# Performance work log

Hardware: AMD Instinct MI355X
Metric: run time of the kernel (lower is better)

The kernel has to match this reference:

```python
import jax, jax.numpy as jnp
import numpy as np

N_PTS = 131072
IN_CH = 63
IN_CH_VIEWS = 27
WIDTH = 256
NUM_HEADS = 4
SCALE = 0.05


def setup_inputs() -> dict:
    key = jax.random.key(0)
    ks = jax.random.split(key, 12)
    H, W = NUM_HEADS, WIDTH
    inp = {
        'x': jax.random.normal(ks[0], (N_PTS, IN_CH + IN_CH_VIEWS), jnp.float32),
        'head_idx': jax.random.randint(ks[1], (N_PTS,), 0, NUM_HEADS),
        # shared trunk: layer0 63->256, layers1..3 256->256 (no skip before split_at=4)
        'W0': jax.random.normal(ks[2], (IN_CH, W), jnp.float32) * SCALE,
        'b0': jnp.zeros((W,), jnp.float32),
        'Ws': jax.random.normal(ks[3], (3, W, W), jnp.float32) * SCALE,
        'bs': jnp.zeros((3, W), jnp.float32),
        # per-head tails: g=4 in skips -> (W+63)->W, then g=5..7 W->W
        'tW0': jax.random.normal(ks[4], (H, W + IN_CH, W), jnp.float32) * SCALE,
        'tb0': jnp.zeros((H, W), jnp.float32),
        'tWs': jax.random.normal(ks[5], (H, 3, W, W), jnp.float32) * SCALE,
        'tbs': jnp.zeros((H, 3, W), jnp.float32),
        # per-head viewdirs output heads
        'featW': jax.random.normal(ks[6], (H, W, W), jnp.float32) * SCALE,
        'featb': jnp.zeros((H, W), jnp.float32),
        'alphaW': jax.random.normal(ks[7], (H, W, 1), jnp.float32) * SCALE,
        'alphab': jnp.zeros((H, 1), jnp.float32),
        'viewsW': jax.random.normal(ks[8], (H, IN_CH_VIEWS + W, W // 2), jnp.float32) * SCALE,
        'viewsb': jnp.zeros((H, W // 2), jnp.float32),
        'rgbW': jax.random.normal(ks[9], (H, W // 2, 3), jnp.float32) * SCALE,
        'rgbb': jnp.zeros((H, 3), jnp.float32),
    }
    return inp


def reference(x, head_idx, W0, b0, Ws, bs, tW0, tb0, tWs, tbs,
              featW, featb, alphaW, alphab, viewsW, viewsb, rgbW, rgbb):
    input_pts = x[:, :IN_CH]          # [N, 63]
    input_views = x[:, IN_CH:]        # [N, 27]

    # shared trunk (layers 0..3, no skip hits in this range)
    h = jax.nn.relu(input_pts @ W0 + b0)
    for i in range(Ws.shape[0]):
        h = jax.nn.relu(h @ Ws[i] + bs[i])

    # per-head tails, computed densely for ALL heads (as in the original)
    # first tail layer g=4 is a skip layer: concat input_pts
    ht = jnp.concatenate([input_pts, h], axis=-1)          # [N, 319]
    ha = jax.nn.relu(jnp.einsum('nf,hfo->nho', ht, tW0) + tb0[None])  # [N, H, 256]
    for j in range(tWs.shape[1]):
        ha = jax.nn.relu(jnp.einsum('nho,hop->nhp', ha, tWs[:, j]) + tbs[None, :, j])

    # per-head viewdir output heads
    alpha = jnp.einsum('nho,hop->nhp', ha, alphaW) + alphab[None]     # [N, H, 1]
    feat = jnp.einsum('nho,hop->nhp', ha, featW) + featb[None]        # [N, H, 256]
    views_b = jnp.broadcast_to(input_views[:, None, :], (x.shape[0], feat.shape[1], IN_CH_VIEWS))
    hv = jnp.concatenate([feat, views_b], axis=-1)                    # [N, H, 283]
    hv = jax.nn.relu(jnp.einsum('nho,hop->nhp', hv, viewsW) + viewsb[None])
    rgb = jnp.einsum('nho,hop->nhp', hv, rgbW) + rgbb[None]           # [N, H, 3]

    outs = jnp.concatenate([rgb, alpha], axis=-1)                     # [N, H, 4]
    sel = jnp.take_along_axis(outs, head_idx[:, None, None], axis=1)[:, 0]  # [N, 4]
    return sel
```

## Files before the change

### kernel.cpp

```cpp
#include <hip/hip_runtime.h>

#define N_PTS 131072
#define TILE 64
#define THREADS 512

typedef __bf16 bf16;
typedef __bf16 bf16x8 __attribute__((ext_vector_type(8)));
typedef float f32x4 __attribute__((ext_vector_type(4)));

#define WS_PERM_OFF   256
#define WS_WPACK_OFF  (256 + N_PTS * 4)
#define OFF_W0     0
#define OFF_WS     16384
#define OFF_TW0    212992
#define OFF_TWS    540672
#define OFF_FEATW  1327104
#define OFF_VIEWSW 1589248
#define TOTAL_PACK 1736704

#define PTS_BASE 0
#define H_BASE   8192
#define LDS_BYTES 40960

__device__ __forceinline__ unsigned swz(unsigned base, unsigned row, unsigned rowstride,
                                        unsigned kbyte) {
  return (base + row * rowstride + kbyte) ^ ((row & 7u) << 4);
}

__global__ void k_pack(const float* __restrict__ W0, const float* __restrict__ Ws,
                       const float* __restrict__ tW0, const float* __restrict__ tWs,
                       const float* __restrict__ featW, const float* __restrict__ viewsW,
                       bf16* __restrict__ out) {
  for (int idx = blockIdx.x * blockDim.x + threadIdx.x; idx < TOTAL_PACK;
       idx += gridDim.x * blockDim.x) {
    float v;
    if (idx < OFF_WS) {
      int o = idx >> 6, k = idx & 63;
      v = (k < 63) ? W0[k * 256 + o] : 0.f;
    } else if (idx < OFF_TW0) {
      int i = idx - OFF_WS; int l = i >> 16, r = i & 65535, o = r >> 8, k = r & 255;
      v = Ws[l * 65536 + k * 256 + o];
    } else if (idx < OFF_TWS) {
      int i = idx - OFF_TW0; int h = i / 81920, r = i % 81920, o = r / 320, k = r % 320;
      v = (k < 63) ? tW0[(h * 319 + k) * 256 + o]
                   : (k == 63 ? 0.f : tW0[(h * 319 + k - 1) * 256 + o]);
    } else if (idx < OFF_FEATW) {
      int i = idx - OFF_TWS; int hj = i >> 16, r = i & 65535, o = r >> 8, k = r & 255;
      v = tWs[(hj * 256 + k) * 256 + o];
    } else if (idx < OFF_VIEWSW) {
      int i = idx - OFF_FEATW; int h = i >> 16, r = i & 65535, o = r >> 8, k = r & 255;
      v = featW[(h * 256 + k) * 256 + o];
    } else {
      int i = idx - OFF_VIEWSW; int h = i / 36864, r = i % 36864, o = r / 288, k = r % 288;
      v = (k < 283) ? viewsW[(h * 283 + k) * 128 + o] : 0.f;
    }
    out[idx] = (bf16)v;
  }
}

__global__ void k_zero(int* c) { if (threadIdx.x < 64) c[threadIdx.x] = 0; }

__global__ void k_count(const int* __restrict__ head, int* __restrict__ c) {
  __shared__ int lc[4];
  if (threadIdx.x < 4) lc[threadIdx.x] = 0;
  __syncthreads();
  int p = blockIdx.x * 256 + threadIdx.x;
  if (p < N_PTS) atomicAdd(&lc[head[p]], 1);
  __syncthreads();
  if (threadIdx.x < 4 && lc[threadIdx.x]) atomicAdd(&c[threadIdx.x], lc[threadIdx.x]);
}

__global__ void k_scan(int* c) {
  c[8] = 0; c[24] = 0;
  for (int h = 0; h < 4; ++h) {
    c[8 + h + 1] = c[8 + h] + c[h];
    c[16 + h] = c[8 + h];
    c[24 + h + 1] = c[24 + h] + (c[h] + TILE - 1) / TILE;
  }
}

__global__ void k_scatter(const int* __restrict__ head, int* __restrict__ c,
                          int* __restrict__ perm) {
  int p = blockIdx.x * 256 + threadIdx.x;
  int h = (p < N_PTS) ? head[p] : -1;
  int lane = threadIdx.x & 63;
  #pragma unroll
  for (int hh = 0; hh < 4; ++hh) {
    unsigned long long m = __ballot(h == hh);
    if (m == 0ull) continue;
    int leader = __builtin_ctzll(m);
    int base = 0;
    if (lane == leader) base = atomicAdd(&c[16 + hh], __popcll(m));
    base = __shfl(base, leader);
    if (h == hh) {
      int rank = __popcll(m & ((1ull << lane) - 1ull));
      perm[base + rank] = p;
    }
  }
}

template <int NFRAG, bool RELU, int A0KC, int A1KC>
__device__ __forceinline__ void mfma_layer(char* lds, const bf16* __restrict__ Wt, int wK,
                                           const float* __restrict__ bias,
                                           int a0_base, int a0_stride,
                                           int a1_base, int a1_stride,
                                           int out_base, int out_stride,
                                           int lane, int wave) {
  const int l15 = lane & 15, l4 = lane >> 4;
  constexpr int KC = A0KC + A1KC;
  f32x4 acc[4][NFRAG];
  #pragma unroll
  for (int m = 0; m < 4; ++m)
    #pragma unroll
    for (int n = 0; n < NFRAG; ++n) acc[m][n] = (f32x4){0.f, 0.f, 0.f, 0.f};

  const int c0 = wave * (NFRAG * 16);
  const bf16* bbase[NFRAG];
  #pragma unroll
  for (int n = 0; n < NFRAG; ++n)
    bbase[n] = Wt + (c0 + n * 16 + l15) * wK + l4 * 8;

  bf16x8 bcur[NFRAG];
  #pragma unroll
  for (int n = 0; n < NFRAG; ++n) bcur[n] = *(const bf16x8*)(bbase[n]);

  #pragma unroll 1
  for (int kc = 0; kc < KC; ++kc) {
    const int kn = (kc + 1 < KC) ? kc + 1 : kc;
    bf16x8 bnext[NFRAG];
    #pragma unroll
    for (int n = 0; n < NFRAG; ++n) bnext[n] = *(const bf16x8*)(bbase[n] + kn * 32);

    const int base   = (kc < A0KC) ? a0_base   : a1_base;
    const int stride = (kc < A0KC) ? a0_stride : a1_stride;
    const int kl     = ((kc < A0KC) ? kc : kc - A0KC) * 32;
    bf16x8 a[4];
    #pragma unroll
    for (int m = 0; m < 4; ++m)
      a[m] = *(const bf16x8*)(lds + swz(base, m * 16 + l15, stride, (kl + l4 * 8) * 2));

    #pragma unroll
    for (int n = 0; n < NFRAG; ++n)
      #pragma unroll
      for (int m = 0; m < 4; ++m)
        acc[m][n] = __builtin_amdgcn_mfma_f32_16x16x32_bf16(a[m], bcur[n], acc[m][n], 0, 0, 0);

    #pragma unroll
    for (int n = 0; n < NFRAG; ++n) bcur[n] = bnext[n];
  }
  __syncthreads();
  #pragma unroll
  for (int n = 0; n < NFRAG; ++n) {
    int col = c0 + n * 16 + l15;
    float bv = bias[col];
    #pragma unroll
    for (int m = 0; m < 4; ++m) {
      #pragma unroll
      for (int j = 0; j < 4; ++j) {
        float v = acc[m][n][j] + bv;
        if (RELU) v = fmaxf(v, 0.f);
        int row = m * 16 + l4 * 4 + j;
        *(bf16*)(lds + swz(out_base, row, out_stride, col * 2)) = (bf16)v;
      }
    }
  }
  __syncthreads();
}

__global__ __launch_bounds__(THREADS, 4) void k_main(
    const float* __restrict__ x, const int* __restrict__ ctrl, const int* __restrict__ perm,
    const bf16* __restrict__ wpack,
    const float* __restrict__ b0, const float* __restrict__ bs,
    const float* __restrict__ tb0p, const float* __restrict__ tbsp,
    const float* __restrict__ featb, const float* __restrict__ alphaW,
    const float* __restrict__ alphab, const float* __restrict__ viewsb,
    const float* __restrict__ rgbW, const float* __restrict__ rgbb,
    float* __restrict__ outp) {
  __shared__ __attribute__((aligned(16))) char lds[LDS_BYTES];
  __shared__ int pidx[TILE];
  __shared__ float alpha_s[TILE];

  const int tid = threadIdx.x;
  const int lane = tid & 63, wave = tid >> 6;

  const int tbA = ctrl[24], tbB = ctrl[25], tbC = ctrl[26], tbD = ctrl[27], tbE = ctrl[28];
  const int bid = blockIdx.x;
  if (bid >= tbE) return;
  const int hh = (bid >= tbB) + (bid >= tbC) + (bid >= tbD);
  const int tb_h = (hh == 0) ? tbA : ((hh == 1) ? tbB : ((hh == 2) ? tbC : tbD));
  const int start = ctrl[8 + hh] + (bid - tb_h) * TILE;
  const int nv = min(TILE, ctrl[8 + hh + 1] - start);

  if (tid < TILE) pidx[tid] = (tid < nv) ? perm[start + tid] : -1;
  __syncthreads();

  for (int i = tid; i < TILE * 64; i += THREADS) {
    int row = i >> 6, c = i & 63;
    int p = pidx[row];
    float v = (p >= 0 && c < 63) ? x[p * 90 + c] : 0.f;
    *(bf16*)(lds + swz(PTS_BASE, row, 128, c * 2)) = (bf16)v;
  }
  __syncthreads();

  const bf16* W0p    = wpack + OFF_W0;
  const bf16* Wsp    = wpack + OFF_WS;
  const bf16* tW0p   = wpack + OFF_TW0 + hh * 81920;
  const bf16* tWsp   = wpack + OFF_TWS + hh * 3 * 65536;
  const bf16* featWp = wpack + OFF_FEATW + hh * 65536;
  const bf16* viewsWp= wpack + OFF_VIEWSW + hh * 36864;

  mfma_layer<2, true, 2, 0>(lds, W0p, 64, b0, PTS_BASE, 128, 0, 0, H_BASE, 512, lane, wave);
  for (int i = 0; i < 3; ++i)
    mfma_layer<2, true, 8, 0>(lds, Wsp + i * 65536, 256, bs + i * 256,
                              H_BASE, 512, 0, 0, H_BASE, 512, lane, wave);
  mfma_layer<2, true, 2, 8>(lds, tW0p, 320, tb0p + hh * 256,
                            PTS_BASE, 128, H_BASE, 512, H_BASE, 512, lane, wave);

  for (int i = tid; i < TILE * 32; i += THREADS) {
    int row = i >> 5, c = i & 31;
    int p = pidx[row];
    float v = (p >= 0 && c < 27) ? x[p * 90 + 63 + c] : 0.f;
    *(bf16*)(lds + swz(PTS_BASE, row, 128, c * 2)) = (bf16)v;
  }

  for (int j = 0; j < 3; ++j)
    mfma_layer<2, true, 8, 0>(lds, tWsp + j * 65536, 256, tbsp + (hh * 3 + j) * 256,
                              H_BASE, 512, 0, 0, H_BASE, 512, lane, wave);

  if (wave < 4) {
    int p = wave * 16 + (lane & 15);
    int kq = lane >> 4;
    const float* aW = alphaW + hh * 256;
    float s = 0.f;
    for (int i = 0; i < 8; ++i) {
      int k = kq * 64 + i * 8;
      bf16x8 hv8 = *(const bf16x8*)(lds + swz(H_BASE, p, 512, k * 2));
      #pragma unroll
      for (int j = 0; j < 8; ++j) s += (float)hv8[j] * aW[k + j];
    }
    s += __shfl_xor(s, 16);
    s += __shfl_xor(s, 32);
    if (kq == 0) alpha_s[p] = s + alphab[hh];
  }
  __syncthreads();

  mfma_layer<2, false, 8, 0>(lds, featWp, 256, featb + hh * 256,
                             H_BASE, 512, 0, 0, H_BASE, 512, lane, wave);
  mfma_layer<1, true, 8, 1>(lds, viewsWp, 288, viewsb + hh * 128,
                            H_BASE, 512, PTS_BASE, 128, H_BASE, 512, lane, wave);

  if (wave < 4) {
    int p = wave * 16 + (lane & 15);
    int kq = lane >> 4;
    const float* rW = rgbW + hh * 128 * 3;
    float r0 = 0.f, r1 = 0.f, r2 = 0.f;
    for (int i = 0; i < 4; ++i) {
      int k = kq * 32 + i * 8;
      bf16x8 hv8 = *(const bf16x8*)(lds + swz(H_BASE, p, 512, k * 2));
      #pragma unroll
      for (int j = 0; j < 8; ++j) {
        float hvf = (float)hv8[j];
        r0 += hvf * rW[(k + j) * 3 + 0];
        r1 += hvf * rW[(k + j) * 3 + 1];
        r2 += hvf * rW[(k + j) * 3 + 2];
      }
    }
    r0 += __shfl_xor(r0, 16); r0 += __shfl_xor(r0, 32);
    r1 += __shfl_xor(r1, 16); r1 += __shfl_xor(r1, 32);
    r2 += __shfl_xor(r2, 16); r2 += __shfl_xor(r2, 32);
    if (kq == 0 && p < nv) {
      int pt = pidx[p];
      float4 o = make_float4(r0 + rgbb[hh * 3 + 0], r1 + rgbb[hh * 3 + 1],
                             r2 + rgbb[hh * 3 + 2], alpha_s[p]);
      *(float4*)(outp + pt * 4) = o;
    }
  }
}

extern "C" void kernel_launch(void* const* d_in, const int* in_sizes, int n_in,
                              void* d_out, int out_size, void* d_ws, size_t ws_size,
                              hipStream_t stream) {
  const float* x      = (const float*)d_in[0];
  const int*   head   = (const int*)d_in[1];
  const float* W0     = (const float*)d_in[2];
  const float* b0     = (const float*)d_in[3];
  const float* Ws     = (const float*)d_in[4];
  const float* bs     = (const float*)d_in[5];
  const float* tW0    = (const float*)d_in[6];
  const float* tb0    = (const float*)d_in[7];
  const float* tWs    = (const float*)d_in[8];
  const float* tbs    = (const float*)d_in[9];
  const float* featW  = (const float*)d_in[10];
  const float* featb  = (const float*)d_in[11];
  const float* alphaW = (const float*)d_in[12];
  const float* alphab = (const float*)d_in[13];
  const float* viewsW = (const float*)d_in[14];
  const float* viewsb = (const float*)d_in[15];
  const float* rgbW   = (const float*)d_in[16];
  const float* rgbb   = (const float*)d_in[17];

  int*  ctrl  = (int*)d_ws;
  int*  perm  = (int*)((char*)d_ws + WS_PERM_OFF);
  bf16* wpack = (bf16*)((char*)d_ws + WS_WPACK_OFF);

  k_pack<<<2048, 256, 0, stream>>>(W0, Ws, tW0, tWs, featW, viewsW, wpack);
  k_zero<<<1, 64, 0, stream>>>(ctrl);
  k_count<<<N_PTS / 256, 256, 0, stream>>>(head, ctrl);
  k_scan<<<1, 1, 0, stream>>>(ctrl);
  k_scatter<<<N_PTS / 256, 256, 0, stream>>>(head, ctrl, perm);
  k_main<<<N_PTS / TILE + 4, THREADS, 0, stream>>>(x, ctrl, perm, wpack,
                                                   b0, bs, tb0, tbs, featb, alphaW, alphab,
                                                   viewsb, rgbW, rgbb, (float*)d_out);
}
```

Before: 470.9 us.

## Ping-pong activation buffers to drop per-layer barrier and deepen weight prefetch

Activations now alternate between two LDS buffers, so each layer reads from one and writes the other. This lets the barrier between the MFMA loop and the epilogue store, plus the one after the alpha pass, be removed. Weight fragment prefetch is deepened from one k-step ahead to two. The zero kernel is folded into the pack kernel to save a launch. LDS use grows from 40 KB to 72 KB per block, which may lower occupancy, and the extra prefetch registers add register pressure.

Result: slower. 568.9 us (+20.8%).

```diff
diff --git a/kernel.cpp b/kernel.cpp
--- a/kernel.cpp
+++ b/kernel.cpp
@@ -19,8 +19,9 @@
 #define TOTAL_PACK 1736704
 
 #define PTS_BASE 0
-#define H_BASE   8192
-#define LDS_BYTES 40960
+#define HA_BASE  8192
+#define HB_BASE  40960
+#define LDS_BYTES 73728
 
 __device__ __forceinline__ unsigned swz(unsigned base, unsigned row, unsigned rowstride,
                                         unsigned kbyte) {
@@ -30,7 +31,8 @@
 __global__ void k_pack(const float* __restrict__ W0, const float* __restrict__ Ws,
                        const float* __restrict__ tW0, const float* __restrict__ tWs,
                        const float* __restrict__ featW, const float* __restrict__ viewsW,
-                       bf16* __restrict__ out) {
+                       bf16* __restrict__ out, int* __restrict__ ctrl) {
+  if (blockIdx.x == 0 && threadIdx.x < 64) ctrl[threadIdx.x] = 0;
   for (int idx = blockIdx.x * blockDim.x + threadIdx.x; idx < TOTAL_PACK;
        idx += gridDim.x * blockDim.x) {
     float v;
@@ -58,8 +60,6 @@
   }
 }
 
-__global__ void k_zero(int* c) { if (threadIdx.x < 64) c[threadIdx.x] = 0; }
-
 __global__ void k_count(const int* __restrict__ head, int* __restrict__ c) {
   __shared__ int lc[4];
   if (threadIdx.x < 4) lc[threadIdx.x] = 0;
@@ -115,21 +115,22 @@
     for (int n = 0; n < NFRAG; ++n) acc[m][n] = (f32x4){0.f, 0.f, 0.f, 0.f};
 
   const int c0 = wave * (NFRAG * 16);
-  const bf16* bbase[NFRAG];
-  #pragma unroll
-  for (int n = 0; n < NFRAG; ++n)
-    bbase[n] = Wt + (c0 + n * 16 + l15) * wK + l4 * 8;
-
-  bf16x8 bcur[NFRAG];
-  #pragma unroll
-  for (int n = 0; n < NFRAG; ++n) bcur[n] = *(const bf16x8*)(bbase[n]);
+  const bf16* bp = Wt + (c0 + l15) * wK + l4 * 8;
+  const int nstep = 16 * wK;
+
+  bf16x8 bc[NFRAG], bn[NFRAG];
+  #pragma unroll
+  for (int n = 0; n < NFRAG; ++n) bc[n] = *(const bf16x8*)(bp + n * nstep);
+  constexpr int K1 = (KC > 1) ? 32 : 0;
+  #pragma unroll
+  for (int n = 0; n < NFRAG; ++n) bn[n] = *(const bf16x8*)(bp + n * nstep + K1);
 
   #pragma unroll 1
   for (int kc = 0; kc < KC; ++kc) {
-    const int kn = (kc + 1 < KC) ? kc + 1 : kc;
-    bf16x8 bnext[NFRAG];
-    #pragma unroll
-    for (int n = 0; n < NFRAG; ++n) bnext[n] = *(const bf16x8*)(bbase[n] + kn * 32);
+    const int kf = (kc + 2 < KC) ? kc + 2 : KC - 1;
+    bf16x8 bf_[NFRAG];
+    #pragma unroll
+    for (int n = 0; n < NFRAG; ++n) bf_[n] = *(const bf16x8*)(bp + n * nstep + kf * 32);
 
     const int base   = (kc < A0KC) ? a0_base   : a1_base;
     const int stride = (kc < A0KC) ? a0_stride : a1_stride;
@@ -143,12 +144,12 @@
     for (int n = 0; n < NFRAG; ++n)
       #pragma unroll
       for (int m = 0; m < 4; ++m)
-        acc[m][n] = __builtin_amdgcn_mfma_f32_16x16x32_bf16(a[m], bcur[n], acc[m][n], 0, 0, 0);
-
-    #pragma unroll
-    for (int n = 0; n < NFRAG; ++n) bcur[n] = bnext[n];
-  }
-  __syncthreads();
+        acc[m][n] = __builtin_amdgcn_mfma_f32_16x16x32_bf16(a[m], bc[n], acc[m][n], 0, 0, 0);
+
+    #pragma unroll
+    for (int n = 0; n < NFRAG; ++n) { bc[n] = bn[n]; bn[n] = bf_[n]; }
+  }
+
   #pragma unroll
   for (int n = 0; n < NFRAG; ++n) {
     int col = c0 + n * 16 + l15;
@@ -209,12 +210,12 @@
   const bf16* featWp = wpack + OFF_FEATW + hh * 65536;
   const bf16* viewsWp= wpack + OFF_VIEWSW + hh * 36864;
 
-  mfma_layer<2, true, 2, 0>(lds, W0p, 64, b0, PTS_BASE, 128, 0, 0, H_BASE, 512, lane, wave);
-  for (int i = 0; i < 3; ++i)
-    mfma_layer<2, true, 8, 0>(lds, Wsp + i * 65536, 256, bs + i * 256,
-                              H_BASE, 512, 0, 0, H_BASE, 512, lane, wave);
+  mfma_layer<2, true, 2, 0>(lds, W0p, 64, b0, PTS_BASE, 128, 0, 0, HA_BASE, 512, lane, wave);
+  mfma_layer<2, true, 8, 0>(lds, Wsp,           256, bs,       HA_BASE, 512, 0, 0, HB_BASE, 512, lane, wave);
+  mfma_layer<2, true, 8, 0>(lds, Wsp + 65536,   256, bs + 256, HB_BASE, 512, 0, 0, HA_BASE, 512, lane, wave);
+  mfma_layer<2, true, 8, 0>(lds, Wsp + 131072,  256, bs + 512, HA_BASE, 512, 0, 0, HB_BASE, 512, lane, wave);
   mfma_layer<2, true, 2, 8>(lds, tW0p, 320, tb0p + hh * 256,
-                            PTS_BASE, 128, H_BASE, 512, H_BASE, 512, lane, wave);
+                            PTS_BASE, 128, HB_BASE, 512, HA_BASE, 512, lane, wave);
 
   for (int i = tid; i < TILE * 32; i += THREADS) {
     int row = i >> 5, c = i & 31;
@@ -223,9 +224,9 @@
     *(bf16*)(lds + swz(PTS_BASE, row, 128, c * 2)) = (bf16)v;
   }
 
-  for (int j = 0; j < 3; ++j)
-    mfma_layer<2, true, 8, 0>(lds, tWsp + j * 65536, 256, tbsp + (hh * 3 + j) * 256,
-                              H_BASE, 512, 0, 0, H_BASE, 512, lane, wave);
+  mfma_layer<2, true, 8, 0>(lds, tWsp,          256, tbsp + hh * 768,       HA_BASE, 512, 0, 0, HB_BASE, 512, lane, wave);
+  mfma_layer<2, true, 8, 0>(lds, tWsp + 65536,  256, tbsp + hh * 768 + 256, HB_BASE, 512, 0, 0, HA_BASE, 512, lane, wave);
+  mfma_layer<2, true, 8, 0>(lds, tWsp + 131072, 256, tbsp + hh * 768 + 512, HA_BASE, 512, 0, 0, HB_BASE, 512, lane, wave);
 
   if (wave < 4) {
     int p = wave * 16 + (lane & 15);
@@ -234,7 +235,7 @@
     float s = 0.f;
     for (int i = 0; i < 8; ++i) {
       int k = kq * 64 + i * 8;
-      bf16x8 hv8 = *(const bf16x8*)(lds + swz(H_BASE, p, 512, k * 2));
+      bf16x8 hv8 = *(const bf16x8*)(lds + swz(HB_BASE, p, 512, k * 2));
       #pragma unroll
       for (int j = 0; j < 8; ++j) s += (float)hv8[j] * aW[k + j];
     }
@@ -242,12 +243,11 @@
     s += __shfl_xor(s, 32);
     if (kq == 0) alpha_s[p] = s + alphab[hh];
   }
-  __syncthreads();
 
   mfma_layer<2, false, 8, 0>(lds, featWp, 256, featb + hh * 256,
-                             H_BASE, 512, 0, 0, H_BASE, 512, lane, wave);
+                             HB_BASE, 512, 0, 0, HA_BASE, 512, lane, wave);
   mfma_layer<1, true, 8, 1>(lds, viewsWp, 288, viewsb + hh * 128,
-                            H_BASE, 512, PTS_BASE, 128, H_BASE, 512, lane, wave);
+                            HA_BASE, 512, PTS_BASE, 128, HB_BASE, 512, lane, wave);
 
   if (wave < 4) {
     int p = wave * 16 + (lane & 15);
@@ -256,7 +256,7 @@
     float r0 = 0.f, r1 = 0.f, r2 = 0.f;
     for (int i = 0; i < 4; ++i) {
       int k = kq * 32 + i * 8;
-      bf16x8 hv8 = *(const bf16x8*)(lds + swz(H_BASE, p, 512, k * 2));
+      bf16x8 hv8 = *(const bf16x8*)(lds + swz(HB_BASE, p, 512, k * 2));
       #pragma unroll
       for (int j = 0; j < 8; ++j) {
         float hvf = (float)hv8[j];
@@ -303,8 +303,7 @@
   int*  perm  = (int*)((char*)d_ws + WS_PERM_OFF);
   bf16* wpack = (bf16*)((char*)d_ws + WS_WPACK_OFF);
 
-  k_pack<<<2048, 256, 0, stream>>>(W0, Ws, tW0, tWs, featW, viewsW, wpack);
-  k_zero<<<1, 64, 0, stream>>>(ctrl);
+  k_pack<<<2048, 256, 0, stream>>>(W0, Ws, tW0, tWs, featW, viewsW, wpack, ctrl);
   k_count<<<N_PTS / 256, 256, 0, stream>>>(head, ctrl);
   k_scan<<<1, 1, 0, stream>>>(ctrl);
   k_scatter<<<N_PTS / 256, 256, 0, stream>>>(head, ctrl, perm);
```

## Stage weight tiles into double-buffered LDS via global_load_lds; fuse head count into pack

Applied to the files above, without the earlier changes.

Each MFMA layer now stages its weight K-slices into a double-buffered LDS region with direct global-to-LDS loads, using an XOR swizzle. Waves read their B fragments from LDS instead of holding prefetched fragments in registers, which removes register-side global loads and register pressure. The cost is a block-wide barrier per K step, and LDS per block grows from 40 KB to 72 KB, which may lower the number of resident blocks per CU. Separately, the head-count pass is folded into the weight-pack kernel and the zero kernel becomes a memset, removing two small launches.

Result: faster. 440.6 us (-6.4%).

```diff
diff --git a/kernel.cpp b/kernel.cpp
--- a/kernel.cpp
+++ b/kernel.cpp
@@ -20,19 +20,32 @@
 
 #define PTS_BASE 0
 #define H_BASE   8192
-#define LDS_BYTES 40960
+#define B_BASE   40960
+#define LDS_BYTES 73728
 
 __device__ __forceinline__ unsigned swz(unsigned base, unsigned row, unsigned rowstride,
                                         unsigned kbyte) {
   return (base + row * rowstride + kbyte) ^ ((row & 7u) << 4);
 }
 
+__device__ __forceinline__ void gload_lds16(const bf16* g, char* l) {
+  __builtin_amdgcn_global_load_lds(
+      (const __attribute__((address_space(1))) void*)g,
+      (__attribute__((address_space(3))) void*)l, 16, 0, 0);
+}
+
 __global__ void k_pack(const float* __restrict__ W0, const float* __restrict__ Ws,
                        const float* __restrict__ tW0, const float* __restrict__ tWs,
                        const float* __restrict__ featW, const float* __restrict__ viewsW,
-                       bf16* __restrict__ out) {
-  for (int idx = blockIdx.x * blockDim.x + threadIdx.x; idx < TOTAL_PACK;
-       idx += gridDim.x * blockDim.x) {
+                       bf16* __restrict__ out, const int* __restrict__ head,
+                       int* __restrict__ ctrl) {
+  __shared__ int lc[4];
+  if (threadIdx.x < 4) lc[threadIdx.x] = 0;
+  __syncthreads();
+  int gid = blockIdx.x * blockDim.x + threadIdx.x;
+  if (gid < N_PTS) atomicAdd(&lc[head[gid]], 1);
+
+  for (int idx = gid; idx < TOTAL_PACK; idx += gridDim.x * blockDim.x) {
     float v;
     if (idx < OFF_WS) {
       int o = idx >> 6, k = idx & 63;
@@ -56,18 +69,8 @@
     }
     out[idx] = (bf16)v;
   }
-}
-
-__global__ void k_zero(int* c) { if (threadIdx.x < 64) c[threadIdx.x] = 0; }
-
-__global__ void k_count(const int* __restrict__ head, int* __restrict__ c) {
-  __shared__ int lc[4];
-  if (threadIdx.x < 4) lc[threadIdx.x] = 0;
-  __syncthreads();
-  int p = blockIdx.x * 256 + threadIdx.x;
-  if (p < N_PTS) atomicAdd(&lc[head[p]], 1);
-  __syncthreads();
-  if (threadIdx.x < 4 && lc[threadIdx.x]) atomicAdd(&c[threadIdx.x], lc[threadIdx.x]);
+  __syncthreads();
+  if (threadIdx.x < 4 && lc[threadIdx.x]) atomicAdd(&ctrl[threadIdx.x], lc[threadIdx.x]);
 }
 
 __global__ void k_scan(int* c) {
@@ -99,7 +102,21 @@
   }
 }
 
-template <int NFRAG, bool RELU, int A0KC, int A1KC>
+template <int OUTS>
+__device__ __forceinline__ void stage_B(const bf16* __restrict__ Wt, int wK, int kk,
+                                        char* lds, int bufsel, int wave, int lane) {
+  constexpr int ISSUES = OUTS / 128;
+  #pragma unroll
+  for (int s = 0; s < ISSUES; ++s) {
+    int reg = wave * ISSUES + s;
+    int o = reg * 16 + (lane >> 2);
+    int j = lane & 3;
+    const bf16* g = Wt + o * wK + kk + ((j ^ (o & 3)) << 3);
+    gload_lds16(g, lds + B_BASE + bufsel * 16384 + reg * 1024);
+  }
+}
+
+template <int NFRAG, bool RELU, int A0KC, int A1KC, int OUTS>
 __device__ __forceinline__ void mfma_layer(char* lds, const bf16* __restrict__ Wt, int wK,
                                            const float* __restrict__ bias,
                                            int a0_base, int a0_stride,
@@ -115,21 +132,14 @@
     for (int n = 0; n < NFRAG; ++n) acc[m][n] = (f32x4){0.f, 0.f, 0.f, 0.f};
 
   const int c0 = wave * (NFRAG * 16);
-  const bf16* bbase[NFRAG];
-  #pragma unroll
-  for (int n = 0; n < NFRAG; ++n)
-    bbase[n] = Wt + (c0 + n * 16 + l15) * wK + l4 * 8;
-
-  bf16x8 bcur[NFRAG];
-  #pragma unroll
-  for (int n = 0; n < NFRAG; ++n) bcur[n] = *(const bf16x8*)(bbase[n]);
+
+  stage_B<OUTS>(Wt, wK, 0, lds, 0, wave, lane);
+  __syncthreads();
 
   #pragma unroll 1
   for (int kc = 0; kc < KC; ++kc) {
-    const int kn = (kc + 1 < KC) ? kc + 1 : kc;
-    bf16x8 bnext[NFRAG];
-    #pragma unroll
-    for (int n = 0; n < NFRAG; ++n) bnext[n] = *(const bf16x8*)(bbase[n] + kn * 32);
+    const int buf = kc & 1;
+    if (kc + 1 < KC) stage_B<OUTS>(Wt, wK, (kc + 1) * 32, lds, buf ^ 1, wave, lane);
 
     const int base   = (kc < A0KC) ? a0_base   : a1_base;
     const int stride = (kc < A0KC) ? a0_stride : a1_stride;
@@ -139,16 +149,22 @@
     for (int m = 0; m < 4; ++m)
       a[m] = *(const bf16x8*)(lds + swz(base, m * 16 + l15, stride, (kl + l4 * 8) * 2));
 
+    bf16x8 b[NFRAG];
+    #pragma unroll
+    for (int n = 0; n < NFRAG; ++n) {
+      int col = c0 + n * 16 + l15;
+      b[n] = *(const bf16x8*)(lds + B_BASE + buf * 16384 + col * 64 + ((l4 ^ (col & 3)) << 4));
+    }
+
     #pragma unroll
     for (int n = 0; n < NFRAG; ++n)
       #pragma unroll
       for (int m = 0; m < 4; ++m)
-        acc[m][n] = __builtin_amdgcn_mfma_f32_16x16x32_bf16(a[m], bcur[n], acc[m][n], 0, 0, 0);
-
-    #pragma unroll
-    for (int n = 0; n < NFRAG; ++n) bcur[n] = bnext[n];
-  }
-  __syncthreads();
+        acc[m][n] = __builtin_amdgcn_mfma_f32_16x16x32_bf16(a[m], b[n], acc[m][n], 0, 0, 0);
+
+    __syncthreads();
+  }
+
   #pragma unroll
   for (int n = 0; n < NFRAG; ++n) {
     int col = c0 + n * 16 + l15;
@@ -164,7 +180,6 @@
       }
     }
   }
-  __syncthreads();
 }
 
 __global__ __launch_bounds__(THREADS, 4) void k_main(
@@ -200,7 +215,6 @@
     float v = (p >= 0 && c < 63) ? x[p * 90 + c] : 0.f;
     *(bf16*)(lds + swz(PTS_BASE, row, 128, c * 2)) = (bf16)v;
   }
-  __syncthreads();
 
   const bf16* W0p    = wpack + OFF_W0;
   const bf16* Wsp    = wpack + OFF_WS;
@@ -209,12 +223,12 @@
   const bf16* featWp = wpack + OFF_FEATW + hh * 65536;
   const bf16* viewsWp= wpack + OFF_VIEWSW + hh * 36864;
 
-  mfma_layer<2, true, 2, 0>(lds, W0p, 64, b0, PTS_BASE, 128, 0, 0, H_BASE, 512, lane, wave);
-  for (int i = 0; i < 3; ++i)
-    mfma_layer<2, true, 8, 0>(lds, Wsp + i * 65536, 256, bs + i * 256,
-                              H_BASE, 512, 0, 0, H_BASE, 512, lane, wave);
-  mfma_layer<2, true, 2, 8>(lds, tW0p, 320, tb0p + hh * 256,
-                            PTS_BASE, 128, H_BASE, 512, H_BASE, 512, lane, wave);
+  mfma_layer<2, true, 2, 0, 256>(lds, W0p, 64, b0, PTS_BASE, 128, 0, 0, H_BASE, 512, lane, wave);
+  mfma_layer<2, true, 8, 0, 256>(lds, Wsp,          256, bs,       H_BASE, 512, 0, 0, H_BASE, 512, lane, wave);
+  mfma_layer<2, true, 8, 0, 256>(lds, Wsp + 65536,  256, bs + 256, H_BASE, 512, 0, 0, H_BASE, 512, lane, wave);
+  mfma_layer<2, true, 8, 0, 256>(lds, Wsp + 131072, 256, bs + 512, H_BASE, 512, 0, 0, H_BASE, 512, lane, wave);
+  mfma_layer<2, true, 2, 8, 256>(lds, tW0p, 320, tb0p + hh * 256,
+                                 PTS_BASE, 128, H_BASE, 512, H_BASE, 512, lane, wave);
 
   for (int i = tid; i < TILE * 32; i += THREADS) {
     int row = i >> 5, c = i & 31;
@@ -223,9 +237,11 @@
     *(bf16*)(lds + swz(PTS_BASE, row, 128, c * 2)) = (bf16)v;
   }
 
-  for (int j = 0; j < 3; ++j)
-    mfma_layer<2, true, 8, 0>(lds, tWsp + j * 65536, 256, tbsp + (hh * 3 + j) * 256,
-                              H_BASE, 512, 0, 0, H_BASE, 512, lane, wave);
+  mfma_layer<2, true, 8, 0, 256>(lds, tWsp,          256, tbsp + hh * 768,       H_BASE, 512, 0, 0, H_BASE, 512, lane, wave);
+  mfma_layer<2, true, 8, 0, 256>(lds, tWsp + 65536,  256, tbsp + hh * 768 + 256, H_BASE, 512, 0, 0, H_BASE, 512, lane, wave);
+  mfma_layer<2, true, 8, 0, 256>(lds, tWsp + 131072, 256, tbsp + hh * 768 + 512, H_BASE, 512, 0, 0, H_BASE, 512, lane, wave);
+
+  __syncthreads();
 
   if (wave < 4) {
     int p = wave * 16 + (lane & 15);
@@ -242,12 +258,13 @@
     s += __shfl_xor(s, 32);
     if (kq == 0) alpha_s[p] = s + alphab[hh];
   }
-  __syncthreads();
-
-  mfma_layer<2, false, 8, 0>(lds, featWp, 256, featb + hh * 256,
-                             H_BASE, 512, 0, 0, H_BASE, 512, lane, wave);
-  mfma_layer<1, true, 8, 1>(lds, viewsWp, 288, viewsb + hh * 128,
-                            H_BASE, 512, PTS_BASE, 128, H_BASE, 512, lane, wave);
+
+  mfma_layer<2, false, 8, 0, 256>(lds, featWp, 256, featb + hh * 256,
+                                  H_BASE, 512, 0, 0, H_BASE, 512, lane, wave);
+  mfma_layer<1, true, 8, 1, 128>(lds, viewsWp, 288, viewsb + hh * 128,
+                                 H_BASE, 512, PTS_BASE, 128, H_BASE, 512, lane, wave);
+
+  __syncthreads();
 
   if (wave < 4) {
     int p = wave * 16 + (lane & 15);
@@ -303,9 +320,8 @@
   int*  perm  = (int*)((char*)d_ws + WS_PERM_OFF);
   bf16* wpack = (bf16*)((char*)d_ws + WS_WPACK_OFF);
 
-  k_pack<<<2048, 256, 0, stream>>>(W0, Ws, tW0, tWs, featW, viewsW, wpack);
-  k_zero<<<1, 64, 0, stream>>>(ctrl);
-  k_count<<<N_PTS / 256, 256, 0, stream>>>(head, ctrl);
+  hipMemsetAsync(ctrl, 0, 256, stream);
+  k_pack<<<2048, 256, 0, stream>>>(W0, Ws, tW0, tWs, featW, viewsW, wpack, head, ctrl);
   k_scan<<<1, 1, 0, stream>>>(ctrl);
   k_scatter<<<N_PTS / 256, 256, 0, stream>>>(head, ctrl, perm);
   k_main<<<N_PTS / TILE + 4, THREADS, 0, stream>>>(x, ctrl, perm, wpack,
```
